# Optimization experiments

Measured on AMD Instinct MI355X. Metric: run time of the kernel, lower is better.

Reference implementation:

```python
import jax, jax.numpy as jnp
import numpy as np

B, N, C = 16, 1024, 768            # N = window_size**2 = 32*32
NUM_HEADS, BANK = 12, 256
HEAD_DIM = C // NUM_HEADS
LN_EPS = 1e-5


def setup_inputs() -> dict:
    key = jax.random.key(0)
    ks = jax.random.split(key, 9)
    s = 0.02
    return {
        "x": jax.random.normal(ks[0], (B, N, C), dtype=jnp.float32),
        "qkv_w": jax.random.normal(ks[1], (3 * C, C), dtype=jnp.float32) * s,
        "qkv_b": jnp.zeros((3 * C,), dtype=jnp.float32),
        "proj_w": jax.random.normal(ks[2], (C, C), dtype=jnp.float32) * s,
        "proj_b": jnp.zeros((C,), dtype=jnp.float32),
        "norm_w": jnp.ones((C,), dtype=jnp.float32),
        "norm_b": jnp.zeros((C,), dtype=jnp.float32),
        "bank_k": jax.random.normal(ks[3], (BANK, C), dtype=jnp.float32) * s,
        "bank_v": jax.random.normal(ks[4], (BANK, C), dtype=jnp.float32) * s,
    }


def _split_heads_bank(bank, b):
    # (BANK, C) -> broadcast to (b, BANK, C) -> (b, H, BANK, D)
    t = jnp.broadcast_to(bank, (b,) + bank.shape)
    return t.reshape(b, BANK, NUM_HEADS, HEAD_DIM).transpose(0, 2, 1, 3)


def reference(x, qkv_w, qkv_b, proj_w, proj_b, norm_w, norm_b, bank_k, bank_v):
    b, n, c = x.shape
    h, d = NUM_HEADS, HEAD_DIM
    # QKV projection: (b, n, 3c) -> (3, b, h, n, d)
    qkv = (jnp.einsum("bnc,fc->bnf", x, qkv_w) + qkv_b)
    qkv = qkv.reshape(b, n, 3, h, d).transpose(2, 0, 3, 1, 4)
    q, k, v = qkv[0], qkv[1], qkv[2]
    # Memory-bank read + concat onto KV
    k_full = jnp.concatenate([k, _split_heads_bank(bank_k, b)], axis=2)  # (b,h,n+BANK,d)
    v_full = jnp.concatenate([v, _split_heads_bank(bank_v, b)], axis=2)
    # SDPA (dropout_p = 0.0)
    scores = jnp.einsum("bhnd,bhmd->bhnm", q, k_full) / jnp.sqrt(jnp.asarray(d, x.dtype))
    attn = jax.nn.softmax(scores, axis=-1)
    out = jnp.einsum("bhnm,bhmd->bhnd", attn, v_full)
    out = out.transpose(0, 2, 1, 3).reshape(b, n, c)
    # Bank write value: LayerNorm(proj(out))  (side effect in torch; returned here)
    p = jnp.einsum("bnc,oc->bno", out, proj_w) + proj_b
    mu = jnp.mean(p, axis=-1, keepdims=True)
    var = jnp.mean(jnp.square(p - mu), axis=-1, keepdims=True)
    bank_update = (p - mu) * jax.lax.rsqrt(var + LN_EPS) * norm_w + norm_b
    return out, bank_update
```

## Files before the change

kernel.cpp:

```cpp
#include <hip/hip_runtime.h>

typedef __attribute__((ext_vector_type(8))) short short8;
typedef __attribute__((ext_vector_type(4))) float float4_t;
typedef unsigned short u16;

#define K_DIM 768

__device__ __forceinline__ u16 f2bf(float f) {
  union { float f; unsigned u; } v; v.f = f;
  unsigned r = v.u + 0x7FFFu + ((v.u >> 16) & 1u);
  return (u16)(r >> 16);
}

__device__ __forceinline__ u16 f2bf_trunc(float f) {
  union { float f; unsigned u; } v; v.f = f;
  return (u16)(v.u >> 16);
}

__device__ __forceinline__ void gload16(const void* g, void* l) {
  __builtin_amdgcn_global_load_lds(
      (__attribute__((address_space(1))) void*)g,
      (__attribute__((address_space(3))) void*)l, 16, 0, 0);
}

__global__ __launch_bounds__(256) void cvt_all_kernel(
    const float* __restrict__ x, const float* __restrict__ qw,
    const float* __restrict__ pw, const float* __restrict__ bkf,
    const float* __restrict__ bvf,
    u16* __restrict__ xbf, u16* __restrict__ qwbf, u16* __restrict__ pwbf,
    u16* __restrict__ bk, u16* __restrict__ bvt) {
  const int blk = blockIdx.x;
  if (blk < 14592) {
    int i = blk * 256 + threadIdx.x;
    const float* src; u16* dst;
    if (i < 3145728)      { src = x;  dst = xbf; }
    else if (i < 3588096) { src = qw; dst = qwbf; i -= 3145728; }
    else                  { src = pw; dst = pwbf; i -= 3588096; }
    float4 v = ((const float4*)src)[i];
    union { u16 h[4]; unsigned long long ll; } o;
    o.h[0] = f2bf(v.x); o.h[1] = f2bf(v.y); o.h[2] = f2bf(v.z); o.h[3] = f2bf(v.w);
    ((unsigned long long*)dst)[i] = o.ll;
  } else {
    int idx = (blk - 14592) * 256 + threadIdx.x;
    int m = idx / 768;
    int c = idx - m * 768;
    int h = c >> 6, d = c & 63;
    bk[(h * 256 + m) * 64 + d] = f2bf(bkf[idx]);
    bvt[(h * 64 + d) * 256 + m] = f2bf(bvf[idx]);
  }
}

template <int MODE>
__global__ __launch_bounds__(256) void gemm128(
    const u16* __restrict__ A, const u16* __restrict__ Bw,
    const float* __restrict__ bias,
    u16* __restrict__ q_ws, u16* __restrict__ k_ws, u16* __restrict__ vt_ws,
    float* __restrict__ p_out) {
  __shared__ u16 As[128 * 32];
  __shared__ u16 Bs[128 * 32];
  const int tid = threadIdx.x;
  const int w = tid >> 6, lane = tid & 63;
  const int l15 = lane & 15, quad = lane >> 4;
  const int wm = w >> 1, wn = w & 1;
  const int bm = blockIdx.y, bn = blockIdx.x;

  float4_t acc[4][4];
#pragma unroll
  for (int i = 0; i < 4; i++)
#pragma unroll
    for (int j = 0; j < 4; j++) acc[i][j] = (float4_t){0.f, 0.f, 0.f, 0.f};

  for (int kt = 0; kt < K_DIM; kt += 32) {
    __syncthreads();
#pragma unroll
    for (int r = 0; r < 2; r++) {
      const int off = (w * 2 + r) * 1024 + lane * 16;
      const int row = off >> 6;
      const int grp = (off & 63) >> 4;
      const int lcol = (grp ^ (row & 3)) * 8;
      gload16(A + (size_t)(bm * 128 + row) * K_DIM + kt + lcol, (char*)As + off);
      gload16(Bw + (size_t)(bn * 128 + row) * K_DIM + kt + lcol, (char*)Bs + off);
    }
    __syncthreads();
    short8 af[4], bfr[4];
#pragma unroll
    for (int mt = 0; mt < 4; mt++) {
      const int row = wm * 64 + mt * 16 + l15;
      af[mt] = *(const short8*)(As + row * 32 + (quad ^ (row & 3)) * 8);
    }
#pragma unroll
    for (int nt = 0; nt < 4; nt++) {
      const int row = wn * 64 + nt * 16 + l15;
      bfr[nt] = *(const short8*)(Bs + row * 32 + (quad ^ (row & 3)) * 8);
    }
#pragma unroll
    for (int mt = 0; mt < 4; mt++)
#pragma unroll
      for (int nt = 0; nt < 4; nt++)
        acc[mt][nt] = __builtin_amdgcn_mfma_f32_16x16x32_bf16(af[mt], bfr[nt], acc[mt][nt], 0, 0, 0);
  }

  const float QS = 0.18033688011112042f;
#pragma unroll
  for (int mt = 0; mt < 4; mt++) {
#pragma unroll
    for (int nt = 0; nt < 4; nt++) {
      const int row0 = bm * 128 + wm * 64 + mt * 16 + quad * 4;
      const int f = bn * 128 + wn * 64 + nt * 16 + l15;
      const float bv = bias[f];
      if (MODE == 0) {
        const int which = f / 768;
        const int rem = f - which * 768;
        const int h = rem >> 6, d = rem & 63;
#pragma unroll
        for (int r2 = 0; r2 < 4; r2++) {
          float v = acc[mt][nt][r2] + bv;
          const int i = row0 + r2;
          const int bb = i >> 10, n = i & 1023;
          const size_t bhh = (size_t)(bb * 12 + h);
          if (which == 0)      q_ws[(bhh * 1024 + n) * 64 + d] = f2bf(v * QS);
          else if (which == 1) k_ws[(bhh * 1024 + n) * 64 + d] = f2bf(v);
          else                 vt_ws[(bhh * 64 + d) * 1024 + n] = f2bf(v);
        }
      } else {
#pragma unroll
        for (int r2 = 0; r2 < 4; r2++) {
          const int i = row0 + r2;
          p_out[(size_t)i * 768 + f] = acc[mt][nt][r2] + bv;
        }
      }
    }
  }
}

__global__ __launch_bounds__(256) void fa_kernel(
    const u16* __restrict__ qws, const u16* __restrict__ kws,
    const u16* __restrict__ vtws, const u16* __restrict__ bk,
    const u16* __restrict__ bvt,
    float* __restrict__ out, u16* __restrict__ obf) {
  __shared__ u16 smem[8192];
  u16* Ks  = smem;
  u16* Vts = smem + 4096;

  const int tid = threadIdx.x;
  const int w = tid >> 6, lane = tid & 63;
  const int l15 = lane & 15, quad = lane >> 4;
  u16* Psw = smem + w * 2048;
  const int bh = blockIdx.x;
  const int b = bh / 12, h = bh - b * 12;
  const int q0 = blockIdx.y * 128 + w * 32;

  short8 qf[2][2];
  {
    const u16* qb = qws + ((size_t)bh * 1024 + q0) * 64;
#pragma unroll
    for (int rt = 0; rt < 2; rt++)
#pragma unroll
      for (int c = 0; c < 2; c++)
        qf[rt][c] = *(const short8*)(qb + (rt * 16 + l15) * 64 + c * 32 + quad * 8);
  }

  const short ONE = (short)0x3F80;
  const short8 onesf = (short8){ONE, ONE, ONE, ONE, ONE, ONE, ONE, ONE};

  float4_t O[2][4];
  float4_t lacc[2];
#pragma unroll
  for (int rt = 0; rt < 2; rt++) {
#pragma unroll
    for (int dt = 0; dt < 4; dt++) O[rt][dt] = (float4_t){0.f, 0.f, 0.f, 0.f};
    lacc[rt] = (float4_t){0.f, 0.f, 0.f, 0.f};
  }

  for (int t = 0; t < 20; t++) {
    const int mb = t * 64;
    __syncthreads();
#pragma unroll
    for (int r = 0; r < 2; r++) {
      const int off = (w * 2 + r) * 1024 + lane * 16;
      const int row = off >> 7;
      const int grp = (off & 127) >> 4;
      const int lcol = (grp ^ (row & 7)) * 8;
      const u16* g = (mb < 1024)
          ? kws + ((size_t)bh * 1024 + mb + row) * 64 + lcol
          : bk + ((size_t)h * 256 + (mb - 1024) + row) * 64 + lcol;
      gload16(g, (char*)Ks + off);
      const u16* g2 = (mb < 1024)
          ? vtws + ((size_t)bh * 64 + row) * 1024 + mb + lcol
          : bvt + ((size_t)h * 64 + row) * 256 + (mb - 1024) + lcol;
      gload16(g2, (char*)Vts + off);
    }
    __syncthreads();

    short8 kf[4][2];
#pragma unroll
    for (int ct = 0; ct < 4; ct++)
#pragma unroll
      for (int c = 0; c < 2; c++) {
        const int row = ct * 16 + l15;
        kf[ct][c] = *(const short8*)(Ks + row * 64 + ((c * 4 + quad) ^ (row & 7)) * 8);
      }

    float4_t S[2][4];
#pragma unroll
    for (int rt = 0; rt < 2; rt++)
#pragma unroll
      for (int ct = 0; ct < 4; ct++) {
        float4_t z = (float4_t){0.f, 0.f, 0.f, 0.f};
        z = __builtin_amdgcn_mfma_f32_16x16x32_bf16(qf[rt][0], kf[ct][0], z, 0, 0, 0);
        S[rt][ct] = __builtin_amdgcn_mfma_f32_16x16x32_bf16(qf[rt][1], kf[ct][1], z, 0, 0, 0);
      }

    short8 vf[4][2];
#pragma unroll
    for (int dt = 0; dt < 4; dt++)
#pragma unroll
      for (int c = 0; c < 2; c++) {
        const int row = dt * 16 + l15;
        vf[dt][c] = *(const short8*)(Vts + row * 64 + ((c * 4 + quad) ^ (row & 7)) * 8);
      }

    __syncthreads();

#pragma unroll
    for (int rt = 0; rt < 2; rt++) {
#pragma unroll
      for (int ct = 0; ct < 4; ct++) {
        const int colg = ct * 2 + (l15 >> 3);
#pragma unroll
        for (int r = 0; r < 4; r++) {
          const float p = __builtin_amdgcn_exp2f(S[rt][ct][r]);
          const int q = rt * 16 + quad * 4 + r;
          Psw[q * 64 + (colg ^ (q & 7)) * 8 + (l15 & 7)] = f2bf_trunc(p);
        }
      }
    }

#pragma unroll
    for (int rt = 0; rt < 2; rt++)
#pragma unroll
      for (int c = 0; c < 2; c++) {
        const int qrow = rt * 16 + l15;
        const short8 pf = *(const short8*)(&Psw[qrow * 64 + (((c * 4 + quad) ^ (qrow & 7)) * 8)]);
#pragma unroll
        for (int dt = 0; dt < 4; dt++)
          O[rt][dt] = __builtin_amdgcn_mfma_f32_16x16x32_bf16(pf, vf[dt][c], O[rt][dt], 0, 0, 0);
        lacc[rt] = __builtin_amdgcn_mfma_f32_16x16x32_bf16(pf, onesf, lacc[rt], 0, 0, 0);
      }
  }

#pragma unroll
  for (int rt = 0; rt < 2; rt++) {
    float rl[4];
#pragma unroll
    for (int r = 0; r < 4; r++) rl[r] = 1.f / lacc[rt][r];
#pragma unroll
    for (int dt = 0; dt < 4; dt++)
#pragma unroll
      for (int r = 0; r < 4; r++) {
        const float v = O[rt][dt][r] * rl[r];
        const int n = q0 + rt * 16 + quad * 4 + r;
        const int d = dt * 16 + l15;
        const size_t idx = ((size_t)b * 1024 + n) * 768 + h * 64 + d;
        out[idx] = v;
        obf[idx] = f2bf(v);
      }
  }
}

__global__ __launch_bounds__(256) void ln_kernel(float* __restrict__ p,
                                                 const float* __restrict__ nw,
                                                 const float* __restrict__ nb) {
  __shared__ float red[2][4];
  const int row = blockIdx.x, tid = threadIdx.x;
  float* pr = p + (size_t)row * 768;
  const float x0 = pr[tid], x1 = pr[tid + 256], x2 = pr[tid + 512];
  float s = x0 + x1 + x2;
  float sq = x0 * x0 + x1 * x1 + x2 * x2;
#pragma unroll
  for (int m = 1; m < 64; m <<= 1) {
    s += __shfl_xor(s, m, 64);
    sq += __shfl_xor(sq, m, 64);
  }
  const int w = tid >> 6;
  if ((tid & 63) == 0) { red[0][w] = s; red[1][w] = sq; }
  __syncthreads();
  s = red[0][0] + red[0][1] + red[0][2] + red[0][3];
  sq = red[1][0] + red[1][1] + red[1][2] + red[1][3];
  const float mean = s * (1.0f / 768.0f);
  const float var = sq * (1.0f / 768.0f) - mean * mean;
  const float rstd = rsqrtf(var + 1e-5f);
  pr[tid]       = (x0 - mean) * rstd * nw[tid]       + nb[tid];
  pr[tid + 256] = (x1 - mean) * rstd * nw[tid + 256] + nb[tid + 256];
  pr[tid + 512] = (x2 - mean) * rstd * nw[tid + 512] + nb[tid + 512];
}

extern "C" void kernel_launch(void* const* d_in, const int* in_sizes, int n_in,
                              void* d_out, int out_size, void* d_ws, size_t ws_size,
                              hipStream_t stream) {
  (void)in_sizes; (void)n_in; (void)out_size; (void)ws_size;
  const float* x      = (const float*)d_in[0];
  const float* qkv_w  = (const float*)d_in[1];
  const float* qkv_b  = (const float*)d_in[2];
  const float* proj_w = (const float*)d_in[3];
  const float* proj_b = (const float*)d_in[4];
  const float* norm_w = (const float*)d_in[5];
  const float* norm_b = (const float*)d_in[6];
  const float* bank_k = (const float*)d_in[7];
  const float* bank_v = (const float*)d_in[8];

  char* ws = (char*)d_ws;
  u16* xbf   = (u16*)(ws + 0);
  u16* obf   = (u16*)(ws + 0);
  u16* qwbf  = (u16*)(ws + 25165824);
  u16* pwbf  = (u16*)(ws + 28704768);
  u16* bkbf  = (u16*)(ws + 29884416);
  u16* bvtbf = (u16*)(ws + 30277632);
  u16* q_ws  = (u16*)(ws + 30670848);
  u16* k_ws  = (u16*)(ws + 55836672);
  u16* vt_ws = (u16*)(ws + 81002496);

  float* out0  = (float*)d_out;
  float* p_out = out0 + 12582912;

  cvt_all_kernel<<<15360, 256, 0, stream>>>(x, qkv_w, proj_w, bank_k, bank_v,
                                            xbf, qwbf, pwbf, bkbf, bvtbf);

  gemm128<0><<<dim3(18, 128), 256, 0, stream>>>(xbf, qwbf, qkv_b, q_ws, k_ws, vt_ws, nullptr);
  fa_kernel<<<dim3(192, 8), 256, 0, stream>>>(q_ws, k_ws, vt_ws, bkbf, bvtbf, out0, obf);
  gemm128<1><<<dim3(6, 128), 256, 0, stream>>>(obf, pwbf, proj_b, nullptr, nullptr, nullptr, p_out);
  ln_kernel<<<16384, 256, 0, stream>>>(p_out, norm_w, norm_b);
}
```

Baseline: 431.7 us.

## Replace 128x128 GEMM with double-buffered 256x256 pipelined MFMA GEMM

Replaces the 128x128 tile, single-buffered, 32-wide-K GEMM with a 256x256 tile, 512-thread kernel. It uses double-buffered 64-wide K LDS staging, interleaves async global-to-LDS loads with quadrant-wise MFMA blocks, and adds explicit waitcnt, barriers and setprio scheduling. Block IDs are remapped so tiles sharing A rows land on the same XCD for L2 reuse. The aim is to hide load latency and raise arithmetic intensity for both the QKV and projection GEMMs. In exchange it brings heavy register pressure (128 accumulators per thread) and fewer blocks for the projection GEMM (192), which may underfill the GPU.

```diff
diff --git a/kernel.cpp b/kernel.cpp
--- a/kernel.cpp
+++ b/kernel.cpp
@@ -50,63 +50,171 @@
   }
 }
 
+
+#define SBAR()                                 \
+  do {                                         \
+    __builtin_amdgcn_sched_barrier(0);         \
+    __builtin_amdgcn_s_barrier();              \
+    __builtin_amdgcn_sched_barrier(0);         \
+  } while (0)
+
+#define VMW2()                                                  \
+  do {                                                          \
+    __builtin_amdgcn_sched_barrier(0);                          \
+    asm volatile("s_waitcnt vmcnt(2)" ::: "memory");            \
+  } while (0)
+
+#define VMW0()                                                  \
+  do {                                                          \
+    __builtin_amdgcn_sched_barrier(0);                          \
+    asm volatile("s_waitcnt vmcnt(0)" ::: "memory");            \
+  } while (0)
+
+#define LDA(B_, MH)                                                            \
+  _Pragma("unroll") for (int m_ = 0; m_ < 4; m_++) {                           \
+    const char* p_ =                                                           \
+        (const char*)As[B_] + ((wm * 128 + (MH) * 64 + m_ * 16) << 7);         \
+    af[m_][0] = *(const short8*)(p_ + ab0);                                    \
+    af[m_][1] = *(const short8*)(p_ + ab1);                                    \
+  }
+
+#define LDB(B_, NH, BF)                                                        \
+  _Pragma("unroll") for (int n_ = 0; n_ < 2; n_++) {                           \
+    const char* p_ =                                                           \
+        (const char*)Bs[B_] + ((wn * 64 + (NH) * 32 + n_ * 16) << 7);          \
+    BF[n_][0] = *(const short8*)(p_ + ab0);                                    \
+    BF[n_][1] = *(const short8*)(p_ + ab1);                                    \
+  }
+
+#define MFMAQ(MH, NH, BF)                                                      \
+  do {                                                                         \
+    __builtin_amdgcn_s_setprio(1);                                             \
+    _Pragma("unroll") for (int m_ = 0; m_ < 4; m_++)                           \
+        _Pragma("unroll") for (int n_ = 0; n_ < 2; n_++) {                     \
+      acc[(MH) * 4 + m_][(NH) * 2 + n_] =                                      \
+          __builtin_amdgcn_mfma_f32_16x16x32_bf16(                             \
+              af[m_][0], BF[n_][0], acc[(MH) * 4 + m_][(NH) * 2 + n_], 0, 0,   \
+              0);                                                              \
+      acc[(MH) * 4 + m_][(NH) * 2 + n_] =                                      \
+          __builtin_amdgcn_mfma_f32_16x16x32_bf16(                             \
+              af[m_][1], BF[n_][1], acc[(MH) * 4 + m_][(NH) * 2 + n_], 0, 0,   \
+              0);                                                              \
+    }                                                                          \
+    __builtin_amdgcn_s_setprio(0);                                             \
+  } while (0)
+
 template <int MODE>
-__global__ __launch_bounds__(256) void gemm128(
+__global__ __launch_bounds__(512, 2) void gemm256(
     const u16* __restrict__ A, const u16* __restrict__ Bw,
     const float* __restrict__ bias,
     u16* __restrict__ q_ws, u16* __restrict__ k_ws, u16* __restrict__ vt_ws,
     float* __restrict__ p_out) {
-  __shared__ u16 As[128 * 32];
-  __shared__ u16 Bs[128 * 32];
+  __shared__ u16 As[2][16384];
+  __shared__ u16 Bs[2][16384];
   const int tid = threadIdx.x;
   const int w = tid >> 6, lane = tid & 63;
   const int l15 = lane & 15, quad = lane >> 4;
-  const int wm = w >> 1, wn = w & 1;
-  const int bm = blockIdx.y, bn = blockIdx.x;
-
-  float4_t acc[4][4];
-#pragma unroll
-  for (int i = 0; i < 4; i++)
+  const int wm = w >> 2, wn = w & 3;
+
+  constexpr int NBN = (MODE == 0) ? 9 : 3;
+  const int bid = blockIdx.x;
+  const int xcd = bid & 7, local = bid >> 3;
+  const int bm = xcd * 8 + local / NBN;
+  const int bn = local % NBN;
+
+  int soff[2], loff[2];
+#pragma unroll
+  for (int r = 0; r < 2; r++) {
+    const int off = r * 8192 + tid * 16;
+    const int row = off >> 7;
+    const int grp = (off & 127) >> 4;
+    soff[r] = row * K_DIM + ((grp ^ (row & 7)) * 8);
+    loff[r] = off;
+  }
+  const u16* Abase = A + (size_t)bm * 256 * K_DIM;
+  const u16* Bbase = Bw + (size_t)bn * 256 * K_DIM;
+
+  auto stg = [&](const u16* g0, u16* l0) {
+    gload16(g0 + soff[0], (char*)l0 + loff[0]);
+    gload16(g0 + soff[1], (char*)l0 + loff[1]);
+  };
+
+  const int ab0 = l15 * 128 + (((0 * 4 + quad) ^ (l15 & 7)) << 4);
+  const int ab1 = l15 * 128 + (((1 * 4 + quad) ^ (l15 & 7)) << 4);
+
+  float4_t acc[8][4];
+#pragma unroll
+  for (int i = 0; i < 8; i++)
 #pragma unroll
     for (int j = 0; j < 4; j++) acc[i][j] = (float4_t){0.f, 0.f, 0.f, 0.f};
 
-  for (int kt = 0; kt < K_DIM; kt += 32) {
-    __syncthreads();
-#pragma unroll
-    for (int r = 0; r < 2; r++) {
-      const int off = (w * 2 + r) * 1024 + lane * 16;
-      const int row = off >> 6;
-      const int grp = (off & 63) >> 4;
-      const int lcol = (grp ^ (row & 3)) * 8;
-      gload16(A + (size_t)(bm * 128 + row) * K_DIM + kt + lcol, (char*)As + off);
-      gload16(Bw + (size_t)(bn * 128 + row) * K_DIM + kt + lcol, (char*)Bs + off);
-    }
-    __syncthreads();
-    short8 af[4], bfr[4];
-#pragma unroll
-    for (int mt = 0; mt < 4; mt++) {
-      const int row = wm * 64 + mt * 16 + l15;
-      af[mt] = *(const short8*)(As + row * 32 + (quad ^ (row & 3)) * 8);
-    }
-#pragma unroll
-    for (int nt = 0; nt < 4; nt++) {
-      const int row = wn * 64 + nt * 16 + l15;
-      bfr[nt] = *(const short8*)(Bs + row * 32 + (quad ^ (row & 3)) * 8);
-    }
-#pragma unroll
-    for (int mt = 0; mt < 4; mt++)
-#pragma unroll
-      for (int nt = 0; nt < 4; nt++)
-        acc[mt][nt] = __builtin_amdgcn_mfma_f32_16x16x32_bf16(af[mt], bfr[nt], acc[mt][nt], 0, 0, 0);
+  short8 af[4][2], bf0[2][2], bf1[2][2];
+
+  stg(Abase, &As[0][0]);
+  stg(Abase + 128 * K_DIM, &As[0][8192]);
+  stg(Bbase, &Bs[0][0]);
+  stg(Bbase + 128 * K_DIM, &Bs[0][8192]);
+  stg(Abase + 64, &As[1][0]);
+  VMW2();
+  SBAR();
+
+#pragma unroll 1
+  for (int g = 0; g < 5; g++) {
+    const int kt_o = g * 128 + 64;
+    const int kt_p = g * 128 + 128;
+    const int kt_q = g * 128 + 192;
+    LDA(0, 0); LDB(0, 0, bf0);
+    stg(Abase + 128 * K_DIM + kt_o, &As[1][8192]);
+    SBAR(); MFMAQ(0, 0, bf0); SBAR();
+    LDB(0, 1, bf1);
+    stg(Bbase + kt_o, &Bs[1][0]);
+    SBAR(); MFMAQ(0, 1, bf1); SBAR();
+    LDA(0, 1);
+    stg(Bbase + 128 * K_DIM + kt_o, &Bs[1][8192]);
+    SBAR(); MFMAQ(1, 1, bf1); SBAR();
+    stg(Abase + kt_p, &As[0][0]);
+    VMW2(); SBAR(); MFMAQ(1, 0, bf0); SBAR();
+    LDA(1, 0); LDB(1, 0, bf0);
+    stg(Abase + 128 * K_DIM + kt_p, &As[0][8192]);
+    SBAR(); MFMAQ(0, 0, bf0); SBAR();
+    LDB(1, 1, bf1);
+    stg(Bbase + kt_p, &Bs[0][0]);
+    SBAR(); MFMAQ(0, 1, bf1); SBAR();
+    LDA(1, 1);
+    stg(Bbase + 128 * K_DIM + kt_p, &Bs[0][8192]);
+    SBAR(); MFMAQ(1, 1, bf1); SBAR();
+    stg(Abase + kt_q, &As[1][0]);
+    VMW2(); SBAR(); MFMAQ(1, 0, bf0); SBAR();
+  }
+
+  {
+    const int kt_o = 704;
+    LDA(0, 0); LDB(0, 0, bf0);
+    stg(Abase + 128 * K_DIM + kt_o, &As[1][8192]);
+    SBAR(); MFMAQ(0, 0, bf0); SBAR();
+    LDB(0, 1, bf1);
+    stg(Bbase + kt_o, &Bs[1][0]);
+    SBAR(); MFMAQ(0, 1, bf1); SBAR();
+    LDA(0, 1);
+    stg(Bbase + 128 * K_DIM + kt_o, &Bs[1][8192]);
+    SBAR(); MFMAQ(1, 1, bf1); SBAR();
+    VMW0(); SBAR(); MFMAQ(1, 0, bf0); SBAR();
+    LDA(1, 0); LDB(1, 0, bf0);
+    SBAR(); MFMAQ(0, 0, bf0); SBAR();
+    LDB(1, 1, bf1);
+    SBAR(); MFMAQ(0, 1, bf1); SBAR();
+    LDA(1, 1);
+    SBAR(); MFMAQ(1, 1, bf1); SBAR();
+    MFMAQ(1, 0, bf0);
   }
 
   const float QS = 0.18033688011112042f;
 #pragma unroll
-  for (int mt = 0; mt < 4; mt++) {
-#pragma unroll
-    for (int nt = 0; nt < 4; nt++) {
-      const int row0 = bm * 128 + wm * 64 + mt * 16 + quad * 4;
-      const int f = bn * 128 + wn * 64 + nt * 16 + l15;
+  for (int mi = 0; mi < 8; mi++) {
+#pragma unroll
+    for (int ni = 0; ni < 4; ni++) {
+      const int row0 = bm * 256 + wm * 128 + mi * 16 + quad * 4;
+      const int f = bn * 256 + wn * 64 + ni * 16 + l15;
       const float bv = bias[f];
       if (MODE == 0) {
         const int which = f / 768;
@@ -114,7 +222,7 @@
         const int h = rem >> 6, d = rem & 63;
 #pragma unroll
         for (int r2 = 0; r2 < 4; r2++) {
-          float v = acc[mt][nt][r2] + bv;
+          float v = acc[mi][ni][r2] + bv;
           const int i = row0 + r2;
           const int bb = i >> 10, n = i & 1023;
           const size_t bhh = (size_t)(bb * 12 + h);
@@ -126,7 +234,7 @@
 #pragma unroll
         for (int r2 = 0; r2 < 4; r2++) {
           const int i = row0 + r2;
-          p_out[(size_t)i * 768 + f] = acc[mt][nt][r2] + bv;
+          p_out[(size_t)i * 768 + f] = acc[mi][ni][r2] + bv;
         }
       }
     }
@@ -326,8 +434,8 @@
   cvt_all_kernel<<<15360, 256, 0, stream>>>(x, qkv_w, proj_w, bank_k, bank_v,
                                             xbf, qwbf, pwbf, bkbf, bvtbf);
 
-  gemm128<0><<<dim3(18, 128), 256, 0, stream>>>(xbf, qwbf, qkv_b, q_ws, k_ws, vt_ws, nullptr);
+  gemm256<0><<<dim3(576), 512, 0, stream>>>(xbf, qwbf, qkv_b, q_ws, k_ws, vt_ws, nullptr);
   fa_kernel<<<dim3(192, 8), 256, 0, stream>>>(q_ws, k_ws, vt_ws, bkbf, bvtbf, out0, obf);
-  gemm128<1><<<dim3(6, 128), 256, 0, stream>>>(obf, pwbf, proj_b, nullptr, nullptr, nullptr, p_out);
+  gemm256<1><<<dim3(192), 512, 0, stream>>>(obf, pwbf, proj_b, nullptr, nullptr, nullptr, p_out);
   ln_kernel<<<16384, 256, 0, stream>>>(p_out, norm_w, norm_b);
 }
```

Measured after the change: 425.7 us. Within noise of the previous version (-1.4%).
